# Optimization experiments

Hardware: AMD Instinct MI355X
Metric: run time of the kernel (lower is better)

The kernel has to match this reference:

```python
import jax, jax.numpy as jnp
import numpy as np

NEG_SLOPE = 0.2


def gatv2_conv(x, src, dst, Wl, bl, Wr, br, att, bias, n_nodes):
    """Single-head GATv2Conv (PyG semantics, add_self_loops=False, no edge_attr)."""
    xl = x @ Wl + bl                      # [N, C]  source-side transform (messages)
    xr = x @ Wr + br                      # [N, C]  target-side transform
    h = jax.nn.leaky_relu(xl[src] + xr[dst], NEG_SLOPE)  # [E, C]
    e = h @ att                           # [E]  attention logits
    # segment softmax over edges grouped by dst
    m = jax.ops.segment_max(e, dst, num_segments=n_nodes)   # [N]
    ex = jnp.exp(e - m[dst])                                 # [E]
    s = jax.ops.segment_sum(ex, dst, num_segments=n_nodes)  # [N]
    alpha = ex / s[dst]                                      # [E]
    out = jax.ops.segment_sum(alpha[:, None] * xl[src], dst, num_segments=n_nodes)
    return out + bias


def setup_inputs() -> dict:
    key = jax.random.key(0)
    ks = jax.random.split(key, 20)
    N, E, D_IN, HID, OUT, D_E = 100000, 1600000, 128, 64, 64, 16
    s = 0.05
    inp = {
        "x": jax.random.normal(ks[0], (N, D_IN), dtype=jnp.float32),
        "edge_index": jax.random.randint(ks[1], (2, E), 0, N, dtype=jnp.int64),
        "edge_attr": jax.random.normal(ks[2], (E, D_E), dtype=jnp.float32),
        # conv1 (GATv2, d_in=128 -> hid=64)
        "Wl1": jax.random.normal(ks[3], (D_IN, HID), dtype=jnp.float32) * s,
        "bl1": jnp.zeros((HID,), jnp.float32),
        "Wr1": jax.random.normal(ks[4], (D_IN, HID), dtype=jnp.float32) * s,
        "br1": jnp.zeros((HID,), jnp.float32),
        "att1": jax.random.normal(ks[5], (HID,), dtype=jnp.float32) * s,
        "bc1": jnp.zeros((HID,), jnp.float32),
        # lin1 residual (128 -> 64)
        "W1": jax.random.normal(ks[6], (D_IN, HID), dtype=jnp.float32) * s,
        "b1": jnp.zeros((HID,), jnp.float32),
        # conv2 (64 -> 64)
        "Wl2": jax.random.normal(ks[7], (HID, OUT), dtype=jnp.float32) * s,
        "bl2": jnp.zeros((OUT,), jnp.float32),
        "Wr2": jax.random.normal(ks[8], (HID, OUT), dtype=jnp.float32) * s,
        "br2": jnp.zeros((OUT,), jnp.float32),
        "att2": jax.random.normal(ks[9], (OUT,), dtype=jnp.float32) * s,
        "bc2": jnp.zeros((OUT,), jnp.float32),
        # lin2 residual (64 -> 64)
        "W2": jax.random.normal(ks[10], (HID, OUT), dtype=jnp.float32) * s,
        "b2": jnp.zeros((OUT,), jnp.float32),
    }
    return inp


def reference(x, edge_index, edge_attr,
              Wl1, bl1, Wr1, br1, att1, bc1, W1, b1,
              Wl2, bl2, Wr2, br2, att2, bc2, W2, b2):
    n_nodes = x.shape[0]
    src, dst = edge_index[0], edge_index[1]
    # edge_attr is accepted by forward() but the convs are called without it -> unused
    h = gatv2_conv(x, src, dst, Wl1, bl1, Wr1, br1, att1, bc1, n_nodes) + (x @ W1 + b1)
    h = jax.nn.relu(h)
    out = gatv2_conv(h, src, dst, Wl2, bl2, Wr2, br2, att2, bc2, n_nodes) + (h @ W2 + b2)
    return out
```

## Files before the change

kernel.cpp:

```cpp
#include <hip/hip_runtime.h>

typedef unsigned short u16;
typedef unsigned int u32;
typedef _Float16 f16;
typedef __attribute__((ext_vector_type(4))) _Float16 f16x4;
typedef __attribute__((ext_vector_type(8))) _Float16 f16x8;
typedef __attribute__((ext_vector_type(4))) float f32x4;
typedef __fp16 hh2 __attribute__((ext_vector_type(2)));

#define BCAP 8192
#define BSH  8

__device__ __forceinline__ u32 pkrtz(float a, float b) {
  hh2 r = __builtin_amdgcn_cvt_pkrtz(a, b);
  union { hh2 h; u32 u; } c; c.h = r; return c.u;
}
__device__ __forceinline__ f16x4 mk4(u32 lo, u32 hi) {
  union { u32 u[2]; f16x4 h; } c; c.u[0] = lo; c.u[1] = hi; return c.h;
}
__device__ __forceinline__ f16x8 mk8(u32 a, u32 b, u32 c_, u32 d) {
  union { u32 u[4]; f16x8 h; } c; c.u[0] = a; c.u[1] = b; c.u[2] = c_; c.u[3] = d; return c.h;
}
__device__ __forceinline__ float fexp2(float x) {
  float r; asm("v_exp_f32 %0, %1" : "=v"(r) : "v"(x)); return r;
}

__global__ void __launch_bounds__(256) k_zero(int* __restrict__ p, int n) {
  int i = threadIdx.x + blockIdx.x * 256;
  if (i < n) p[i] = 0;
}

__global__ void __launch_bounds__(256) k_front1(
    const float* __restrict__ Wl1, const float* __restrict__ bl1,
    const float* __restrict__ Wr1, const float* __restrict__ br1,
    const float* __restrict__ W1,  const float* __restrict__ b1,
    const float* __restrict__ Wl2, const float* __restrict__ bl2,
    const float* __restrict__ Wr2, const float* __restrict__ br2,
    const float* __restrict__ W2,  const float* __restrict__ b2,
    f16* __restrict__ Wf1, f16* __restrict__ Wf2,
    float* __restrict__ bias1, float* __restrict__ bias2,
    const int* __restrict__ ei, int* __restrict__ fillA, u32* __restrict__ pairs,
    int E, int NB, int GP)
{
  __shared__ int sm[1024];
  int b = blockIdx.x;
  int t = threadIdx.x;
  if (b < GP) {
    int g = b * 256 + t;
    const int NP1 = 12 * 4 * 64 * 8;
    const int NP2 = 12 * 2 * 64 * 8;
    if (g < NP1) {
      int j = g & 7, l = (g >> 3) & 63, s = (g >> 9) & 3, tt = g >> 11;
      int k = s * 32 + ((l >> 4) << 3) + j;
      int c = tt * 16 + (l & 15);
      const float* W = (c < 64) ? Wl1 : (c < 128 ? Wr1 : W1);
      Wf1[g] = (f16)W[k * 64 + (c & 63)];
    } else if (g < NP1 + NP2) {
      int g2 = g - NP1;
      int j = g2 & 7, l = (g2 >> 3) & 63, s = (g2 >> 9) & 1, tt = g2 >> 10;
      int k = s * 32 + ((l >> 4) << 3) + j;
      int c = tt * 16 + (l & 15);
      const float* W = (c < 64) ? Wl2 : (c < 128 ? Wr2 : W2);
      Wf2[g2] = (f16)W[k * 64 + (c & 63)];
    } else if (g < NP1 + NP2 + 192) {
      int c = g - NP1 - NP2;
      bias1[c] = (c < 64) ? bl1[c] : (c < 128 ? br1[c - 64] : b1[c - 128]);
    } else if (g < NP1 + NP2 + 384) {
      int c = g - NP1 - NP2 - 192;
      bias2[c] = (c < 64) ? bl2[c] : (c < 128 ? br2[c - 64] : b2[c - 128]);
    }
  } else {
    int* lhist = sm;
    int* lbase = sm + 512;
    int c0 = (b - GP) * 8192;
    int n = E - c0; if (n > 8192) n = 8192;
    for (int i = t; i < NB; i += 256) lhist[i] = 0;
    __syncthreads();
    for (int i = t; i < n; i += 256)
      atomicAdd(&lhist[ei[E + c0 + i] >> BSH], 1);
    __syncthreads();
    for (int i = t; i < NB; i += 256) {
      int h = lhist[i];
      lbase[i] = h ? atomicAdd(&fillA[i], h) : 0;
      lhist[i] = 0;
    }
    __syncthreads();
    for (int i = t; i < n; i += 256) {
      int s = ei[c0 + i], d = ei[E + c0 + i];
      int bk = d >> BSH;
      int pos = lbase[bk] + atomicAdd(&lhist[bk], 1);
      if (pos < BCAP) pairs[(size_t)bk * BCAP + pos] = ((u32)s << 8) | (u32)(d & 255);
    }
  }
}

__global__ void __launch_bounds__(256) k_front2(
    const float* __restrict__ X, const f16* __restrict__ Wfrag, const float* __restrict__ bias,
    f16* __restrict__ O0, f16* __restrict__ O1, f16* __restrict__ O2, int N, int GG,
    const u32* __restrict__ pairs, const int* __restrict__ fillA,
    u32* __restrict__ srcs, int* __restrict__ offs, int NB, int E)
{
  __shared__ __align__(16) char smraw[49152];
  int b = blockIdx.x;
  int t = threadIdx.x;
  if (b < GG) {
    constexpr int KS = 4, K = 128;
    f16* wl = (f16*)smraw;
    {
      const int4* src = (const int4*)Wfrag;
      int4* dst = (int4*)wl;
      const int n16 = 12 * KS * 64;
      for (int i = t; i < n16; i += 256) dst[i] = src[i];
    }
    __syncthreads();
    int lane = t & 63, w = t >> 6;
    int g8 = ((lane >> 4) << 3);
    int r16 = b * 64 + w * 16;
    int rowA = r16 + (lane & 15);
    int rowAc = rowA < N ? rowA : N - 1;
    int colc = lane & 15;
    f32x4 acc[12];
#pragma unroll
    for (int tt = 0; tt < 12; ++tt) {
      float bb_ = bias[tt * 16 + colc];
      f32x4 tmp = {bb_, bb_, bb_, bb_};
      acc[tt] = tmp;
    }
#pragma unroll
    for (int s = 0; s < KS; ++s) {
      const float* xp = X + (size_t)rowAc * K + s * 32 + g8;
      float4 x0 = *(const float4*)xp;
      float4 x1 = *(const float4*)(xp + 4);
      f16x8 a = mk8(pkrtz(x0.x, x0.y), pkrtz(x0.z, x0.w),
                    pkrtz(x1.x, x1.y), pkrtz(x1.z, x1.w));
#pragma unroll
      for (int tt = 0; tt < 12; ++tt) {
        f16x8 bb_ = *(const f16x8*)&wl[((tt * KS + s) * 64 + lane) * 8];
        acc[tt] = __builtin_amdgcn_mfma_f32_16x16x32_f16(a, bb_, acc[tt], 0, 0, 0);
      }
    }
    int rowD0 = r16 + ((lane >> 4) << 2);
#pragma unroll
    for (int tt = 0; tt < 12; ++tt) {
      f16* O = (tt < 4) ? O0 : (tt < 8 ? O1 : O2);
      int c = (tt & 3) * 16 + colc;
#pragma unroll
      for (int q = 0; q < 4; ++q) {
        int r = rowD0 + q;
        if (r < N) O[(size_t)r * 64 + c] = (f16)acc[tt][q];
      }
    }
  } else {
    int* cnt   = (int*)smraw;
    int* lfill = cnt + 256;
    int* ps    = lfill + 256;
    int* lsrc  = ps + 256;
    int bk = b - GG;
    int a0 = (2 * t < NB) ? fillA[2 * t] : 0;
    int a1 = (2 * t + 1 < NB) ? fillA[2 * t + 1] : 0;
    ps[t] = a0 + a1;
    __syncthreads();
    for (int d = 1; d < 256; d <<= 1) {
      int x = (t >= d) ? ps[t - d] : 0;
      __syncthreads();
      ps[t] += x;
      __syncthreads();
    }
    int pi = bk >> 1;
    int base = (pi ? ps[pi - 1] : 0) + ((bk & 1) ? fillA[bk & ~1] : 0);
    int m = fillA[bk];
    int n0 = bk << BSH;
    if (bk == 0 && t == 0) offs[N] = E;
    const u32* P = pairs + (size_t)bk * BCAP;
    cnt[t] = 0;
    __syncthreads();
    for (int i = t; i < m; i += 256)
      atomicAdd(&cnt[P[i] & 255], 1);
    __syncthreads();
    int v = cnt[t];
    lfill[t] = v;
    __syncthreads();
    for (int d = 1; d < 256; d <<= 1) {
      int a = (t >= d) ? lfill[t - d] : 0;
      __syncthreads();
      lfill[t] += a;
      __syncthreads();
    }
    int excl = lfill[t] - v;
    if (n0 + t < N) offs[n0 + t] = base + excl;
    __syncthreads();
    lfill[t] = excl;
    __syncthreads();
    for (int i = t; i < m; i += 256) {
      u32 p = P[i];
      int pos = atomicAdd(&lfill[p & 255], 1);
      lsrc[pos] = (int)(((p & 15u) << 28) | (p >> 8));
    }
    __syncthreads();
    for (int i = t; i < m; i += 256) srcs[base + i] = (u32)lsrc[i];
  }
}

__global__ void __launch_bounds__(256) k_gemm2(const f16* __restrict__ Xv,
    const f16* __restrict__ Wfrag, const float* __restrict__ bias,
    f16* __restrict__ O0, f16* __restrict__ O1, f16* __restrict__ O2, int N)
{
  constexpr int KS = 2, K = 64;
  __shared__ f16 wl[12 * KS * 64 * 8];
  const int tid = threadIdx.x;
  {
    const int4* src = (const int4*)Wfrag;
    int4* dst = (int4*)wl;
    const int n16 = 12 * KS * 64;
    for (int i = tid; i < n16; i += 256) dst[i] = src[i];
  }
  __syncthreads();
  int lane = tid & 63, w = tid >> 6;
  int g8 = ((lane >> 4) << 3);
  int r16 = blockIdx.x * 64 + w * 16;
  int rowA = r16 + (lane & 15);
  int rowAc = rowA < N ? rowA : N - 1;
  int colc = lane & 15;
  f32x4 acc[12];
#pragma unroll
  for (int t = 0; t < 12; ++t) {
    float b = bias[t * 16 + colc];
    f32x4 tmp = {b, b, b, b};
    acc[t] = tmp;
  }
#pragma unroll
  for (int s = 0; s < KS; ++s) {
    f16x8 a = *(const f16x8*)(Xv + (size_t)rowAc * K + s * 32 + g8);
#pragma unroll
    for (int t = 0; t < 12; ++t) {
      f16x8 b = *(const f16x8*)&wl[((t * KS + s) * 64 + lane) * 8];
      acc[t] = __builtin_amdgcn_mfma_f32_16x16x32_f16(a, b, acc[t], 0, 0, 0);
    }
  }
  int rowD0 = r16 + ((lane >> 4) << 2);
#pragma unroll
  for (int t = 0; t < 12; ++t) {
    f16* O = (t < 4) ? O0 : (t < 8 ? O1 : O2);
    int c = (t & 3) * 16 + colc;
#pragma unroll
    for (int q = 0; q < 4; ++q) {
      int r = rowD0 + q;
      if (r < N) O[(size_t)r * 64 + c] = (f16)acc[t][q];
    }
  }
}

__global__ void __launch_bounds__(256) k_conv(const int* __restrict__ offs, const u32* __restrict__ srcs,
    const f16* __restrict__ XL, const f16* __restrict__ XR,
    const float* __restrict__ ATT, const float* __restrict__ BC,
    const f16* __restrict__ RES, f16* __restrict__ OH, float* __restrict__ OF,
    int N, int ntiles, int nwaves)
{
  int lane = threadIdx.x & 63, w = threadIdx.x >> 6;
  int g = lane >> 4, c16 = lane & 15;
  int wid = blockIdx.x * 4 + w;

  const float LOG2E = 1.4426950408889634f;
  f16x8 attf0, attf1, Ia, Ib;
#pragma unroll
  for (int j = 0; j < 8; ++j) {
    attf0[j] = (f16)(ATT[g * 8 + j] * LOG2E);
    attf1[j] = (f16)(ATT[32 + g * 8 + j] * LOG2E);
    Ia[j] = (f16)((g * 8 + j == c16) ? 1.f : 0.f);
    Ib[j] = (f16)((g * 8 + j == c16 + 16) ? 1.f : 0.f);
  }
  float bc4[4];
#pragma unroll
  for (int b = 0; b < 4; ++b) bc4[b] = BC[b * 16 + c16];
  const f16 one = (f16)1.f;
  const f16x4 ones = {one, one, one, one};

  for (int tile = wid; tile < ntiles; tile += nwaves) {
    int n0 = tile << 4;
    int nhi = n0 + 16; if (nhi > N) nhi = N;
    int e0 = __builtin_amdgcn_readfirstlane(offs[n0]);
    int e1 = __builtin_amdgcn_readfirstlane(offs[nhi]);
    int cnt = e1 - e0;

    f32x4 agg0 = {0.f, 0.f, 0.f, 0.f}, agg1 = agg0, agg2 = agg0, agg3 = agg0;
    f32x4 den = agg0;

    if (cnt > 0) {
      int ei0 = e0 + lane;
      u32 my = srcs[ei0 < e1 ? ei0 : e0];
      for (int base = 0; base < cnt; base += 64) {
        u32 my_nxt = my;
        if (base + 64 < cnt) {
          int ein = e0 + base + 64 + lane;
          my_nxt = srcs[ein < e1 ? ein : e0];
        }
        int nrem = cnt - base; if (nrem > 64) nrem = 64;
        for (int bb_ = 0; bb_ < nrem; bb_ += 16) {
          u32 vA = __shfl((int)my, bb_ + c16);
          int sA = (int)(vA & 0x0FFFFFFFu);
          int dA = (int)(vA >> 28);
          const f16* rp = XL + (size_t)sA * 64;
          f16x8 x0 = *(const f16x8*)(rp + g * 8);
          f16x8 x1 = *(const f16x8*)(rp + 32 + g * 8);
          const f16* xp = XR + (size_t)(n0 + dA) * 64;
          f16x8 xr0 = *(const f16x8*)(xp + g * 8);
          f16x8 xr1 = *(const f16x8*)(xp + 32 + g * 8);

          f16x8 t0 = x0 + xr0, t1 = x1 + xr1;
          t0 = __builtin_elementwise_max(t0, t0 * (f16)0.2f);
          t1 = __builtin_elementwise_max(t1, t1 * (f16)0.2f);
          f32x4 dot = {0.f, 0.f, 0.f, 0.f};
          dot = __builtin_amdgcn_mfma_f32_16x16x32_f16(t0, attf0, dot, 0, 0, 0);
          dot = __builtin_amdgcn_mfma_f32_16x16x32_f16(t1, attf1, dot, 0, 0, 0);

          f32x4 d0 = {0.f, 0.f, 0.f, 0.f}, d1 = d0, d2 = d0, d3 = d0;
          d0 = __builtin_amdgcn_mfma_f32_16x16x32_f16(x0, Ia, d0, 0, 0, 0);
          d1 = __builtin_amdgcn_mfma_f32_16x16x32_f16(x0, Ib, d1, 0, 0, 0);
          d2 = __builtin_amdgcn_mfma_f32_16x16x32_f16(x1, Ia, d2, 0, 0, 0);
          d3 = __builtin_amdgcn_mfma_f32_16x16x32_f16(x1, Ib, d3, 0, 0, 0);

          float q0, q1, q2, q3;
          {
            u32 v0 = __shfl((int)my, bb_ + g * 4 + 0);
            u32 v1 = __shfl((int)my, bb_ + g * 4 + 1);
            u32 v2 = __shfl((int)my, bb_ + g * 4 + 2);
            u32 v3 = __shfl((int)my, bb_ + g * 4 + 3);
            int eb = base + bb_ + g * 4;
            q0 = ((int)(v0 >> 28) == c16 && eb + 0 < cnt) ? fexp2(dot[0]) : 0.f;
            q1 = ((int)(v1 >> 28) == c16 && eb + 1 < cnt) ? fexp2(dot[1]) : 0.f;
            q2 = ((int)(v2 >> 28) == c16 && eb + 2 < cnt) ? fexp2(dot[2]) : 0.f;
            q3 = ((int)(v3 >> 28) == c16 && eb + 3 < cnt) ? fexp2(dot[3]) : 0.f;
          }
          f16x4 pa  = mk4(pkrtz(q0, q1), pkrtz(q2, q3));
          f16x4 bv0 = mk4(pkrtz(d0[0], d0[1]), pkrtz(d0[2], d0[3]));
          f16x4 bv1 = mk4(pkrtz(d1[0], d1[1]), pkrtz(d1[2], d1[3]));
          f16x4 bv2 = mk4(pkrtz(d2[0], d2[1]), pkrtz(d2[2], d2[3]));
          f16x4 bv3 = mk4(pkrtz(d3[0], d3[1]), pkrtz(d3[2], d3[3]));

          agg0 = __builtin_amdgcn_mfma_f32_16x16x16f16(pa, bv0, agg0, 0, 0, 0);
          agg1 = __builtin_amdgcn_mfma_f32_16x16x16f16(pa, bv1, agg1, 0, 0, 0);
          agg2 = __builtin_amdgcn_mfma_f32_16x16x16f16(pa, bv2, agg2, 0, 0, 0);
          agg3 = __builtin_amdgcn_mfma_f32_16x16x16f16(pa, bv3, agg3, 0, 0, 0);
          den  = __builtin_amdgcn_mfma_f32_16x16x16f16(pa, ones, den, 0, 0, 0);
        }
        my = my_nxt;
      }
    }

    int rowx = n0 + c16; if (rowx >= N) rowx = N - 1;
    const f16* rsp = RES + (size_t)rowx * 64;
    f16x8 rr0 = *(const f16x8*)(rsp + g * 8);
    f16x8 rr1 = *(const f16x8*)(rsp + 32 + g * 8);
    f32x4 r0 = {0.f, 0.f, 0.f, 0.f}, r1 = r0, r2 = r0, r3 = r0;
    r0 = __builtin_amdgcn_mfma_f32_16x16x32_f16(rr0, Ia, r0, 0, 0, 0);
    r1 = __builtin_amdgcn_mfma_f32_16x16x32_f16(rr0, Ib, r1, 0, 0, 0);
    r2 = __builtin_amdgcn_mfma_f32_16x16x32_f16(rr1, Ia, r2, 0, 0, 0);
    r3 = __builtin_amdgcn_mfma_f32_16x16x32_f16(rr1, Ib, r3, 0, 0, 0);

#pragma unroll
    for (int q = 0; q < 4; ++q) {
      int node = n0 + g * 4 + q;
      if (node >= N) break;
      float dv = den[q];
      float rden = dv > 0.f ? 1.f / dv : 0.f;
#pragma unroll
      for (int b = 0; b < 4; ++b) {
        float av = (b == 0) ? agg0[q] : (b == 1) ? agg1[q] : (b == 2) ? agg2[q] : agg3[q];
        float rv = (b == 0) ? r0[q]   : (b == 1) ? r1[q]   : (b == 2) ? r2[q]   : r3[q];
        float o = av * rden + bc4[b] + rv;
        if (OH) { o = fmaxf(o, 0.f); OH[(size_t)node * 64 + b * 16 + c16] = (f16)o; }
        else    { OF[(size_t)node * 64 + b * 16 + c16] = o; }
      }
    }
  }
}

extern "C" void kernel_launch(void* const* d_in, const int* in_sizes, int n_in,
                              void* d_out, int out_size, void* d_ws, size_t ws_size,
                              hipStream_t stream) {
  const float* x   = (const float*)d_in[0];
  const int*   ei  = (const int*)d_in[1];
  const float* Wl1 = (const float*)d_in[3];
  const float* bl1 = (const float*)d_in[4];
  const float* Wr1 = (const float*)d_in[5];
  const float* br1 = (const float*)d_in[6];
  const float* att1= (const float*)d_in[7];
  const float* bc1 = (const float*)d_in[8];
  const float* W1  = (const float*)d_in[9];
  const float* b1  = (const float*)d_in[10];
  const float* Wl2 = (const float*)d_in[11];
  const float* bl2 = (const float*)d_in[12];
  const float* Wr2 = (const float*)d_in[13];
  const float* br2 = (const float*)d_in[14];
  const float* att2= (const float*)d_in[15];
  const float* bc2 = (const float*)d_in[16];
  const float* W2  = (const float*)d_in[17];
  const float* b2  = (const float*)d_in[18];

  const int N = in_sizes[0] / 128;
  const int E = in_sizes[1] / 2;
  const int NB = (N + 255) >> BSH;

  char* base = (char*)d_ws;
  size_t off = 0;
  auto take = [&](size_t bytes) -> void* {
    void* p = base + off;
    off = (off + bytes + 255) & ~(size_t)255;
    return p;
  };
  int* fillA = (int*)take((size_t)NB * 4);
  int* offs  = (int*)take((size_t)(N + 1) * 4);
  u32* pairs = (u32*)take((size_t)NB * BCAP * 4);
  u32* srcs  = (u32*)take((size_t)E * 4);
  f16* Wf1   = (f16*)take(12 * 4 * 64 * 8 * 2);
  f16* Wf2   = (f16*)take(12 * 2 * 64 * 8 * 2);
  float* bias1 = (float*)take(192 * 4);
  float* bias2 = (float*)take(192 * 4);
  f16* xl  = (f16*)take((size_t)N * 64 * 2);
  f16* xr  = (f16*)take((size_t)N * 64 * 2);
  f16* rs  = (f16*)take((size_t)N * 64 * 2);
  f16* h   = (f16*)take((size_t)N * 64 * 2);

  k_zero<<<(NB + 255) / 256, 256, 0, stream>>>(fillA, NB);

  const int prepN = 12 * 4 * 64 * 8 + 12 * 2 * 64 * 8 + 384;
  const int GP = (prepN + 255) / 256;
  const int GA = (E + 8191) / 8192;
  k_front1<<<GP + GA, 256, 0, stream>>>(Wl1, bl1, Wr1, br1, W1, b1,
                                        Wl2, bl2, Wr2, br2, W2, b2,
                                        Wf1, Wf2, bias1, bias2,
                                        ei, fillA, pairs, E, NB, GP);

  const int GG = (N + 63) / 64;
  k_front2<<<GG + NB, 256, 0, stream>>>(x, Wf1, bias1, xl, xr, rs, N, GG,
                                        pairs, fillA, srcs, offs, NB, E);

  const int ntiles = (N + 15) / 16;
  const int CB = 1563, CW = CB * 4;
  k_conv<<<CB, 256, 0, stream>>>(offs, srcs, xl, xr, att1, bc1, rs, h, nullptr, N, ntiles, CW);
  k_gemm2<<<GG, 256, 0, stream>>>(h, Wf2, bias2, xl, xr, rs, N);
  k_conv<<<CB, 256, 0, stream>>>(offs, srcs, xl, xr, att2, bc2, rs, nullptr, (float*)d_out, N, ntiles, CW);
}
```

Baseline: 191.4 us.

## Software-pipeline edge gathers three batches ahead of MFMA compute

```diff
diff --git a/kernel.cpp b/kernel.cpp
--- a/kernel.cpp
+++ b/kernel.cpp
@@ -286,65 +286,81 @@
     f32x4 den = agg0;
 
     if (cnt > 0) {
-      int ei0 = e0 + lane;
-      u32 my = srcs[ei0 < e1 ? ei0 : e0];
-      for (int base = 0; base < cnt; base += 64) {
-        u32 my_nxt = my;
-        if (base + 64 < cnt) {
-          int ein = e0 + base + 64 + lane;
-          my_nxt = srcs[ein < e1 ? ein : e0];
-        }
-        int nrem = cnt - base; if (nrem > 64) nrem = 64;
-        for (int bb_ = 0; bb_ < nrem; bb_ += 16) {
-          u32 vA = __shfl((int)my, bb_ + c16);
-          int sA = (int)(vA & 0x0FFFFFFFu);
-          int dA = (int)(vA >> 28);
-          const f16* rp = XL + (size_t)sA * 64;
-          f16x8 x0 = *(const f16x8*)(rp + g * 8);
-          f16x8 x1 = *(const f16x8*)(rp + 32 + g * 8);
-          const f16* xp = XR + (size_t)(n0 + dA) * 64;
-          f16x8 xr0 = *(const f16x8*)(xp + g * 8);
-          f16x8 xr1 = *(const f16x8*)(xp + 32 + g * 8);
-
-          f16x8 t0 = x0 + xr0, t1 = x1 + xr1;
-          t0 = __builtin_elementwise_max(t0, t0 * (f16)0.2f);
-          t1 = __builtin_elementwise_max(t1, t1 * (f16)0.2f);
-          f32x4 dot = {0.f, 0.f, 0.f, 0.f};
-          dot = __builtin_amdgcn_mfma_f32_16x16x32_f16(t0, attf0, dot, 0, 0, 0);
-          dot = __builtin_amdgcn_mfma_f32_16x16x32_f16(t1, attf1, dot, 0, 0, 0);
-
-          f32x4 d0 = {0.f, 0.f, 0.f, 0.f}, d1 = d0, d2 = d0, d3 = d0;
-          d0 = __builtin_amdgcn_mfma_f32_16x16x32_f16(x0, Ia, d0, 0, 0, 0);
-          d1 = __builtin_amdgcn_mfma_f32_16x16x32_f16(x0, Ib, d1, 0, 0, 0);
-          d2 = __builtin_amdgcn_mfma_f32_16x16x32_f16(x1, Ia, d2, 0, 0, 0);
-          d3 = __builtin_amdgcn_mfma_f32_16x16x32_f16(x1, Ib, d3, 0, 0, 0);
-
-          float q0, q1, q2, q3;
-          {
-            u32 v0 = __shfl((int)my, bb_ + g * 4 + 0);
-            u32 v1 = __shfl((int)my, bb_ + g * 4 + 1);
-            u32 v2 = __shfl((int)my, bb_ + g * 4 + 2);
-            u32 v3 = __shfl((int)my, bb_ + g * 4 + 3);
-            int eb = base + bb_ + g * 4;
-            q0 = ((int)(v0 >> 28) == c16 && eb + 0 < cnt) ? fexp2(dot[0]) : 0.f;
-            q1 = ((int)(v1 >> 28) == c16 && eb + 1 < cnt) ? fexp2(dot[1]) : 0.f;
-            q2 = ((int)(v2 >> 28) == c16 && eb + 2 < cnt) ? fexp2(dot[2]) : 0.f;
-            q3 = ((int)(v3 >> 28) == c16 && eb + 3 < cnt) ? fexp2(dot[3]) : 0.f;
-          }
-          f16x4 pa  = mk4(pkrtz(q0, q1), pkrtz(q2, q3));
-          f16x4 bv0 = mk4(pkrtz(d0[0], d0[1]), pkrtz(d0[2], d0[3]));
-          f16x4 bv1 = mk4(pkrtz(d1[0], d1[1]), pkrtz(d1[2], d1[3]));
-          f16x4 bv2 = mk4(pkrtz(d2[0], d2[1]), pkrtz(d2[2], d2[3]));
-          f16x4 bv3 = mk4(pkrtz(d3[0], d3[1]), pkrtz(d3[2], d3[3]));
-
-          agg0 = __builtin_amdgcn_mfma_f32_16x16x16f16(pa, bv0, agg0, 0, 0, 0);
-          agg1 = __builtin_amdgcn_mfma_f32_16x16x16f16(pa, bv1, agg1, 0, 0, 0);
-          agg2 = __builtin_amdgcn_mfma_f32_16x16x16f16(pa, bv2, agg2, 0, 0, 0);
-          agg3 = __builtin_amdgcn_mfma_f32_16x16x16f16(pa, bv3, agg3, 0, 0, 0);
-          den  = __builtin_amdgcn_mfma_f32_16x16x16f16(pa, ones, den, 0, 0, 0);
-        }
-        my = my_nxt;
-      }
+      int nb = (cnt + 15) >> 4;
+      u32 my = 0;
+      f16x8 Ax0, Ax1, Ar0, Ar1; u32 Adp = 0;
+      f16x8 Bx0, Bx1, Br0, Br1; u32 Bdp = 0;
+      f16x8 Cx0, Cx1, Cr0, Cr1; u32 Cdp = 0;
+
+#define PREFETCH(Px0, Px1, Pr0, Pr1, Pdp, k)                                    \
+      if ((k) < nb) {                                                           \
+        if (((k) & 3) == 0) {                                                   \
+          int ein = e0 + ((k) << 4) + lane;                                     \
+          my = srcs[ein < e1 ? ein : e1 - 1];                                   \
+        }                                                                       \
+        int nw_ = (k) & 3;                                                      \
+        u32 vA = __shfl((int)my, (nw_ << 4) + c16);                             \
+        const f16* rp = XL + (size_t)(vA & 0x0FFFFFFFu) * 64;                   \
+        Px0 = *(const f16x8*)(rp + g * 8);                                      \
+        Px1 = *(const f16x8*)(rp + 32 + g * 8);                                 \
+        const f16* xp = XR + (size_t)(n0 + (int)(vA >> 28)) * 64;               \
+        Pr0 = *(const f16x8*)(xp + g * 8);                                      \
+        Pr1 = *(const f16x8*)(xp + 32 + g * 8);                                 \
+        u32 w0 = __shfl((int)my, (nw_ << 4) + g * 4 + 0);                       \
+        u32 w1 = __shfl((int)my, (nw_ << 4) + g * 4 + 1);                       \
+        u32 w2 = __shfl((int)my, (nw_ << 4) + g * 4 + 2);                       \
+        u32 w3 = __shfl((int)my, (nw_ << 4) + g * 4 + 3);                       \
+        Pdp = (w0 >> 28) | ((w1 >> 28) << 4) | ((w2 >> 28) << 8) | ((w3 >> 28) << 12); \
+      }
+
+#define COMPUTE(Px0, Px1, Pr0, Pr1, Pdp, fb)                                    \
+      {                                                                         \
+        f16x8 t0 = Px0 + Pr0, t1 = Px1 + Pr1;                                   \
+        t0 = __builtin_elementwise_max(t0, t0 * (f16)0.2f);                     \
+        t1 = __builtin_elementwise_max(t1, t1 * (f16)0.2f);                     \
+        f32x4 dot = {0.f, 0.f, 0.f, 0.f};                                       \
+        dot = __builtin_amdgcn_mfma_f32_16x16x32_f16(t0, attf0, dot, 0, 0, 0);  \
+        dot = __builtin_amdgcn_mfma_f32_16x16x32_f16(t1, attf1, dot, 0, 0, 0);  \
+        f32x4 d0 = {0.f, 0.f, 0.f, 0.f}, d1 = d0, d2 = d0, d3 = d0;             \
+        d0 = __builtin_amdgcn_mfma_f32_16x16x32_f16(Px0, Ia, d0, 0, 0, 0);      \
+        d1 = __builtin_amdgcn_mfma_f32_16x16x32_f16(Px0, Ib, d1, 0, 0, 0);      \
+        d2 = __builtin_amdgcn_mfma_f32_16x16x32_f16(Px1, Ia, d2, 0, 0, 0);      \
+        d3 = __builtin_amdgcn_mfma_f32_16x16x32_f16(Px1, Ib, d3, 0, 0, 0);      \
+        int eb = ((fb) << 4) + g * 4;                                           \
+        float q0 = ((int)((Pdp >>  0) & 15u) == c16 && eb + 0 < cnt) ? fexp2(dot[0]) : 0.f; \
+        float q1 = ((int)((Pdp >>  4) & 15u) == c16 && eb + 1 < cnt) ? fexp2(dot[1]) : 0.f; \
+        float q2 = ((int)((Pdp >>  8) & 15u) == c16 && eb + 2 < cnt) ? fexp2(dot[2]) : 0.f; \
+        float q3 = ((int)((Pdp >> 12) & 15u) == c16 && eb + 3 < cnt) ? fexp2(dot[3]) : 0.f; \
+        f16x4 pa  = mk4(pkrtz(q0, q1), pkrtz(q2, q3));                          \
+        f16x4 bv0 = mk4(pkrtz(d0[0], d0[1]), pkrtz(d0[2], d0[3]));              \
+        f16x4 bv1 = mk4(pkrtz(d1[0], d1[1]), pkrtz(d1[2], d1[3]));              \
+        f16x4 bv2 = mk4(pkrtz(d2[0], d2[1]), pkrtz(d2[2], d2[3]));              \
+        f16x4 bv3 = mk4(pkrtz(d3[0], d3[1]), pkrtz(d3[2], d3[3]));              \
+        agg0 = __builtin_amdgcn_mfma_f32_16x16x16f16(pa, bv0, agg0, 0, 0, 0);   \
+        agg1 = __builtin_amdgcn_mfma_f32_16x16x16f16(pa, bv1, agg1, 0, 0, 0);   \
+        agg2 = __builtin_amdgcn_mfma_f32_16x16x16f16(pa, bv2, agg2, 0, 0, 0);   \
+        agg3 = __builtin_amdgcn_mfma_f32_16x16x16f16(pa, bv3, agg3, 0, 0, 0);   \
+        den  = __builtin_amdgcn_mfma_f32_16x16x16f16(pa, ones, den, 0, 0, 0);   \
+      }
+
+      PREFETCH(Ax0, Ax1, Ar0, Ar1, Adp, 0)
+      PREFETCH(Bx0, Bx1, Br0, Br1, Bdp, 1)
+      PREFETCH(Cx0, Cx1, Cr0, Cr1, Cdp, 2)
+
+      int fb = 0;
+      for (; fb + 3 <= nb; fb += 3) {
+        COMPUTE(Ax0, Ax1, Ar0, Ar1, Adp, fb)
+        PREFETCH(Ax0, Ax1, Ar0, Ar1, Adp, fb + 3)
+        COMPUTE(Bx0, Bx1, Br0, Br1, Bdp, fb + 1)
+        PREFETCH(Bx0, Bx1, Br0, Br1, Bdp, fb + 4)
+        COMPUTE(Cx0, Cx1, Cr0, Cr1, Cdp, fb + 2)
+        PREFETCH(Cx0, Cx1, Cr0, Cr1, Cdp, fb + 5)
+      }
+      int rem = nb - fb;
+      if (rem > 0) COMPUTE(Ax0, Ax1, Ar0, Ar1, Adp, fb)
+      if (rem > 1) COMPUTE(Bx0, Bx1, Br0, Br1, Bdp, fb + 1)
+#undef PREFETCH
+#undef COMPUTE
     }
 
     int rowx = n0 + c16; if (rowx >= N) rowx = N - 1;
```

After: 206.8 us. 8.0% more time.
